# Performance work log

Measured on AMD Instinct MI355X. Metric: run time of the kernel, lower is better.

Reference implementation:

```python
import jax, jax.numpy as jnp
import numpy as np

T, B, IN, H = 512, 64, 256, 1024
LN_EPS = 1e-5


def _uniform(key, shape, fan_in):
    bound = 1.0 / np.sqrt(fan_in)
    return jax.random.uniform(key, shape, jnp.float32, -bound, bound)


def setup_inputs() -> dict:
    key = jax.random.key(0)
    ks = jax.random.split(key, 8)
    return {
        "x": jax.random.normal(ks[0], (T, B, IN), jnp.float32),
        "Wproj": _uniform(ks[1], (IN, H), IN),          # input_projection (no bias)
        "Wx0": _uniform(ks[2], (IN, 4 * H), IN),        # layer-0 input weights
        "Wh0": _uniform(ks[3], (H, 4 * H), H),          # layer-0 hidden weights
        "b0": _uniform(ks[4], (4 * H,), H),             # combined input+hidden bias
        "Wx1": _uniform(ks[5], (H, 4 * H), H),
        "Wh1": _uniform(ks[6], (H, 4 * H), H),
        "b1": _uniform(ks[7], (4 * H,), H),
        # per-layer LayerNorm params: [num_layers=2, H]
        "lnc_g": jnp.ones((2, H), jnp.float32), "lnc_b": jnp.zeros((2, H), jnp.float32),
        "lnh_g": jnp.ones((2, H), jnp.float32), "lnh_b": jnp.zeros((2, H), jnp.float32),
        "lno_g": jnp.ones((2, H), jnp.float32), "lno_b": jnp.zeros((2, H), jnp.float32),
    }


def _ln(v, g, b):
    m = jnp.mean(v, axis=-1, keepdims=True)
    var = jnp.mean((v - m) ** 2, axis=-1, keepdims=True)
    return (v - m) * jax.lax.rsqrt(var + LN_EPS) * g + b


def reference(x, Wproj, Wx0, Wh0, b0, Wx1, Wh1, b1,
              lnc_g, lnc_b, lnh_g, lnh_b, lno_g, lno_b):
    def cell(inp, h, c, Wx, Wh, bias, l):
        gates = inp @ Wx + h @ Wh + bias            # [B, 4H]
        i, f, g, o = jnp.split(gates, 4, axis=-1)
        c = jax.nn.sigmoid(f) * c + jnp.exp(i) * jnp.tanh(g)  # exponential input gate
        c = _ln(c, lnc_g[l], lnc_b[l])
        h = jax.nn.sigmoid(o) * jnp.tanh(c)
        h = _ln(h, lnh_g[l], lnh_b[l])
        return h, c

    def step(carry, xt):
        h0, c0, h1, c1 = carry
        # layer 0: cell -> residual (projected input) -> outer LayerNorm
        h0, c0 = cell(xt, h0, c0, Wx0, Wh0, b0, 0)
        h0 = _ln(h0 + xt @ Wproj, lno_g[0], lno_b[0])
        # layer 1: cell -> identity residual -> outer LayerNorm
        h1, c1 = cell(h0, h1, c1, Wx1, Wh1, b1, 1)
        h1 = _ln(h1 + h0, lno_g[1], lno_b[1])
        return (h0, c0, h1, c1), h1

    z = jnp.zeros((x.shape[1], H), x.dtype)
    (h0, c0, h1, c1), output = jax.lax.scan(step, (z, z, z, z), x)
    h_final = jnp.stack([h0, h1])  # [num_layers, B, H]
    c_final = jnp.stack([c0, c1])
    return output, h_final, c_final
```

## Files before the change

kernel.cpp:

```cpp
#include <hip/hip_runtime.h>
#include <math.h>

#define TSTEPS 512
#define BSZ    64
#define INDIM  256
#define HDIM   1024
#define G4     4096
#define NX     5120
#define LN_EPS 1e-5f

#define NBLK   256
#define NTHR   1024
#define CHUNK  8
#define CROWS  (CHUNK * BSZ)
#define NCHUNK (TSTEPS / CHUNK)
#define HRING  16
#define HSLOT  65536

#define LDS_LDK    2054
#define LDS_LO_OFF (16 * LDS_LDK)
#define LDS_W_BYTES (2 * 16 * LDS_LDK * 2)
#define LDS_STG_OFF LDS_W_BYTES
#define LDS_RED_OFF (LDS_W_BYTES + 4096)
#define LDS_BYTES   (LDS_W_BYTES + 4096 + 256)

typedef short          s8v __attribute__((ext_vector_type(8)));
typedef float          f4v __attribute__((ext_vector_type(4)));
typedef unsigned short u16;

#define MFMA __builtin_amdgcn_mfma_f32_16x16x32_bf16

__device__ __forceinline__ u16 f2bf(float f) {
    unsigned u = __float_as_uint(f);
    u += 0x7FFFu + ((u >> 16) & 1u);
    return (u16)(u >> 16);
}
__device__ __forceinline__ float bf2f(u16 h) {
    return __uint_as_float(((unsigned)h) << 16);
}
__device__ __forceinline__ float sigm(float x) { return 1.f / (1.f + expf(-x)); }

__device__ __forceinline__ float aldf(const float* p) {
    unsigned v = __hip_atomic_load((unsigned*)p, __ATOMIC_RELAXED,
                                   __HIP_MEMORY_SCOPE_AGENT);
    return __uint_as_float(v);
}
__device__ __forceinline__ void astf(float* p, float v) {
    __hip_atomic_store((unsigned*)p, __float_as_uint(v), __ATOMIC_RELAXED,
                       __HIP_MEMORY_SCOPE_AGENT);
}
__device__ __forceinline__ void ast16B(u16* p, s8v v) {
    asm volatile("global_store_dwordx4 %0, %1, off sc1"
                 :: "v"(p), "v"(v) : "memory");
}

#define GSTRIDE 512
__device__ __forceinline__ void grid_barrier(int* bar, int nbar, bool fence)
{
    asm volatile("s_waitcnt vmcnt(0)" ::: "memory");
    __syncthreads();
    if (threadIdx.x == 0) {
        const int blk = blockIdx.x;
        const int g   = blk & 15;
        int* gctr = bar + g * GSTRIDE;
        int* ggo  = gctr + 32;
        int* root = bar + 16 * GSTRIDE;
        int v = __hip_atomic_fetch_add(gctr, 1, __ATOMIC_RELAXED,
                                       __HIP_MEMORY_SCOPE_AGENT);
        if (v == nbar * 16 - 1)
            __hip_atomic_fetch_add(root, 1, __ATOMIC_RELAXED,
                                   __HIP_MEMORY_SCOPE_AGENT);
        if (blk < 16) {
            while (__hip_atomic_load(root, __ATOMIC_RELAXED,
                                     __HIP_MEMORY_SCOPE_AGENT) < nbar * 16) {}
            __hip_atomic_store(ggo, nbar, __ATOMIC_RELAXED,
                               __HIP_MEMORY_SCOPE_AGENT);
        } else {
            while (__hip_atomic_load(ggo, __ATOMIC_RELAXED,
                                     __HIP_MEMORY_SCOPE_AGENT) < nbar) {}
        }
        if (fence)
            __builtin_amdgcn_fence(__ATOMIC_ACQUIRE, "agent");
        asm volatile("" ::: "memory");
    }
    __syncthreads();
}

__device__ __forceinline__ void taskA(int g, int lane,
    const u16* __restrict__ h0hi_s, const u16* __restrict__ h0lo_s,
    const u16* __restrict__ Whthi, const u16* __restrict__ Whtlo,
    float* __restrict__ parts0)
{
    const int ks = g & 1, tile = g >> 1;
    const int rt = tile & 3, ct = tile >> 2;
    const int row = lane & 15, kg = lane >> 4;
    const int m = rt * 16 + row;
    const u16* wh = Whthi + (size_t)(ct * 16 + row) * HDIM + ks * 512 + kg * 8;
    const u16* wl = Whtlo + (size_t)(ct * 16 + row) * HDIM + ks * 512 + kg * 8;
    const u16* ah = h0hi_s + (size_t)m * HDIM + ks * 512 + kg * 8;
    const u16* al = h0lo_s + (size_t)m * HDIM + ks * 512 + kg * 8;
    f4v acc = {0.f, 0.f, 0.f, 0.f};
    s8v Ah = *(const s8v*)(ah);
    s8v Al = *(const s8v*)(al);
    s8v Bh = *(const s8v*)(wh);
    s8v Bl = *(const s8v*)(wl);
#pragma unroll
    for (int i = 0; i < 16; ++i) {
        s8v nAh, nAl, nBh, nBl;
        if (i + 1 < 16) {
            const int kn = (i + 1) * 32;
            nAh = *(const s8v*)(ah + kn);
            nAl = *(const s8v*)(al + kn);
            nBh = *(const s8v*)(wh + kn);
            nBl = *(const s8v*)(wl + kn);
        }
        acc = MFMA(Ah, Bh, acc, 0, 0, 0);
        acc = MFMA(Ah, Bl, acc, 0, 0, 0);
        acc = MFMA(Al, Bh, acc, 0, 0, 0);
        Ah = nAh; Al = nAl; Bh = nBh; Bl = nBl;
    }
    float* Cp = parts0 + (size_t)ks * BSZ * G4;
#pragma unroll
    for (int r = 0; r < 4; ++r)
        astf(&Cp[(size_t)(rt * 16 + kg * 4 + r) * G4 + ct * 16 + row], acc[r]);
}

__device__ __forceinline__ void taskX(int task, int c, int lane,
    const u16* __restrict__ xhi, const u16* __restrict__ xlo,
    const u16* __restrict__ Wxthi, const u16* __restrict__ Wxtlo,
    float* __restrict__ xgbuf)
{
    const int mt = task & 31, ct = task >> 5;
    const int row = lane & 15, kg = lane >> 4;
    const int mr = mt * 16 + row;
    const u16* ah = xhi + ((size_t)c * CROWS + mr) * INDIM + kg * 8;
    const u16* al = xlo + ((size_t)c * CROWS + mr) * INDIM + kg * 8;
    const u16* wh = Wxthi + (size_t)(ct * 16 + row) * INDIM + kg * 8;
    const u16* wl = Wxtlo + (size_t)(ct * 16 + row) * INDIM + kg * 8;
    f4v acc = {0.f, 0.f, 0.f, 0.f};
    s8v Ah = *(const s8v*)(ah);
    s8v Al = *(const s8v*)(al);
    s8v Bh = *(const s8v*)(wh);
    s8v Bl = *(const s8v*)(wl);
#pragma unroll
    for (int i = 0; i < 8; ++i) {
        s8v nAh, nAl, nBh, nBl;
        if (i + 1 < 8) {
            const int kn = (i + 1) * 32;
            nAh = *(const s8v*)(ah + kn);
            nAl = *(const s8v*)(al + kn);
            nBh = *(const s8v*)(wh + kn);
            nBl = *(const s8v*)(wl + kn);
        }
        acc = MFMA(Ah, Bh, acc, 0, 0, 0);
        acc = MFMA(Ah, Bl, acc, 0, 0, 0);
        acc = MFMA(Al, Bh, acc, 0, 0, 0);
        Ah = nAh; Al = nAl; Bh = nBh; Bl = nBl;
    }
#pragma unroll
    for (int r = 0; r < 4; ++r)
        astf(&xgbuf[(size_t)(mt * 16 + kg * 4 + r) * NX + ct * 16 + row], acc[r]);
}

__device__ __forceinline__ void taskC(int blk, int wv, int lane,
    const u16* __restrict__ shW,
    const u16* __restrict__ h0hi_s, const u16* __restrict__ h0lo_s,
    const u16* __restrict__ h1hi_s, const u16* __restrict__ h1lo_s,
    float* __restrict__ parts1)
{
    const int rt = wv & 3, hs = wv >> 2;
    const int row = lane & 15, kg = lane >> 4;
    const int m = rt * 16 + row;
    const u16* ah0 = (hs ? h1hi_s : h0hi_s) + (size_t)m * HDIM + kg * 8;
    const u16* al0 = (hs ? h1lo_s : h0lo_s) + (size_t)m * HDIM + kg * 8;
    const u16* sh  = shW + row * LDS_LDK + hs * 1024 + kg * 8;
    const u16* sl  = shW + LDS_LO_OFF + row * LDS_LDK + hs * 1024 + kg * 8;
    f4v acc = {0.f, 0.f, 0.f, 0.f};
    s8v Ah = *(const s8v*)(ah0);
    s8v Al = *(const s8v*)(al0);
#pragma unroll
    for (int i = 0; i < 32; ++i) {
        s8v nAh, nAl;
        if (i + 1 < 32) {
            nAh = *(const s8v*)(ah0 + (i + 1) * 32);
            nAl = *(const s8v*)(al0 + (i + 1) * 32);
        }
        const int kloc = i * 32;
        s8v Bh = *(const s8v*)(sh + kloc);
        s8v Bl = *(const s8v*)(sl + kloc);
        acc = MFMA(Ah, Bh, acc, 0, 0, 0);
        acc = MFMA(Ah, Bl, acc, 0, 0, 0);
        acc = MFMA(Al, Bh, acc, 0, 0, 0);
        Ah = nAh; Al = nAl;
    }
    float* Cp = parts1 + (size_t)hs * BSZ * G4;
#pragma unroll
    for (int r = 0; r < 4; ++r)
        astf(&Cp[(size_t)(rt * 16 + kg * 4 + r) * G4 + blk * 16 + row], acc[r]);
}

__device__ __forceinline__ float2 blk_sum2(float s, float q, float* red, int tid)
{
#pragma unroll
    for (int off = 32; off; off >>= 1) {
        s += __shfl_down(s, off);
        q += __shfl_down(q, off);
    }
    if ((tid & 63) == 0) { red[(tid >> 6) * 2] = s; red[(tid >> 6) * 2 + 1] = q; }
    __syncthreads();
    float ts = 0.f, tq = 0.f;
#pragma unroll
    for (int i = 0; i < 16; ++i) { ts += red[2 * i]; tq += red[2 * i + 1]; }
    __syncthreads();
    return make_float2(ts, tq);
}

__device__ __forceinline__ float lnorm(float v, float2 sq, float g, float b)
{
    float mean = sq.x * (1.f / 1024.f);
    float var  = sq.y * (1.f / 1024.f) - mean * mean;
    return (v - mean) * rsqrtf(var + LN_EPS) * g + b;
}

__device__ __forceinline__ void store_h_16B(u16* stg, int tid,
                                            u16 hi, u16 lo,
                                            u16* dhi, u16* dlo, int base)
{
    stg[tid] = hi;
    stg[1024 + tid] = lo;
    __syncthreads();
    if (tid < 256) {
        const u16* src = stg + (tid >> 7) * 1024 + (tid & 127) * 8;
        s8v v = *(const s8v*)src;
        u16* dst = ((tid >> 7) == 0 ? dhi : dlo) + base + (tid & 127) * 8;
        ast16B(dst, v);
    }
    __syncthreads();
}

__global__ __launch_bounds__(NTHR, 4) void persistent(
    const u16* __restrict__ xhi,  const u16* __restrict__ xlo,
    const u16* __restrict__ Whthi, const u16* __restrict__ Whtlo,
    const u16* __restrict__ Wxthi, const u16* __restrict__ Wxtlo,
    const u16* __restrict__ W1thi, const u16* __restrict__ W1tlo,
    const float* __restrict__ b0, const float* __restrict__ b1,
    const float* __restrict__ lncg, const float* __restrict__ lncb,
    const float* __restrict__ lnhg, const float* __restrict__ lnhb,
    const float* __restrict__ lnog, const float* __restrict__ lnob,
    float* __restrict__ xg,
    float* __restrict__ parts0,
    float* __restrict__ parts1,
    u16* __restrict__ h0hi, u16* __restrict__ h0lo,
    u16* __restrict__ h1hi, u16* __restrict__ h1lo,
    float* __restrict__ out, int* bar)
{
    extern __shared__ char smem[];
    u16*   shW = (u16*)smem;
    u16*   stg = (u16*)(smem + LDS_STG_OFF);
    float* red = (float*)(smem + LDS_RED_OFF);

    const int blk  = blockIdx.x;
    const int tid  = threadIdx.x;
    const int wv   = tid >> 6;
    const int lane = tid & 63;
    int nbar = 0;

    float c0reg = 0.f, h0reg = 0.f, c1reg = 0.f, h1reg = 0.f;

    {
        const size_t gcol = (size_t)(blk * 16 + wv) * 2048;
        for (int j = lane * 8; j < 2048; j += 512) {
            *(s8v*)(shW + wv * LDS_LDK + j)              = *(const s8v*)(W1thi + gcol + j);
            *(s8v*)(shW + LDS_LO_OFF + wv * LDS_LDK + j) = *(const s8v*)(W1tlo + gcol + j);
        }
    }
    grid_barrier(bar, ++nbar, false);

    {
        const int g = blk * 16 + wv;
        for (int task = g; task < 10240; task += 4096)
            taskX(task, 0, lane, xhi, xlo, Wxthi, Wxtlo, xg);
    }
    grid_barrier(bar, ++nbar, false);

    for (int t = 0; t < TSTEPS; ++t) {
        const int s0  = t & (HRING - 1);
        const int s0p = (t - 1) & (HRING - 1);
        const int s1p = (t - 1) & (HRING - 1);
        const bool fence = ((t & 7) == 7);

        if (blk < 64) {
            const int b = blk, n = tid;
            const float* XG = xg + (size_t)((t >> 3) & 1) * CROWS * NX
                                 + (size_t)((t & 7) * BSZ + b) * NX;
            const float* P0 = parts0 + (size_t)b * G4;
            const float* P1 = parts0 + (size_t)(BSZ + b) * G4;
            float gi = aldf(&XG[n])        + aldf(&P0[n])        + aldf(&P1[n])        + b0[n];
            float gf = aldf(&XG[1024 + n]) + aldf(&P0[1024 + n]) + aldf(&P1[1024 + n]) + b0[1024 + n];
            float gg = aldf(&XG[2048 + n]) + aldf(&P0[2048 + n]) + aldf(&P1[2048 + n]) + b0[2048 + n];
            float go = aldf(&XG[3072 + n]) + aldf(&P0[3072 + n]) + aldf(&P1[3072 + n]) + b0[3072 + n];
            float xp = aldf(&XG[4096 + n]);
            float cv = sigm(gf) * c0reg + expf(gi) * tanhf(gg);
            float2 r = blk_sum2(cv, cv * cv, red, tid);
            float cl = lnorm(cv, r, lncg[n], lncb[n]);
            c0reg = cl;
            float hv = sigm(go) * tanhf(cl);
            r = blk_sum2(hv, hv * hv, red, tid);
            float hl = lnorm(hv, r, lnhg[n], lnhb[n]) + xp;
            r = blk_sum2(hl, hl * hl, red, tid);
            float hn = lnorm(hl, r, lnog[n], lnob[n]);
            h0reg = hn;
            u16 hi = f2bf(hn);
            store_h_16B(stg, tid, hi, f2bf(hn - bf2f(hi)),
                        h0hi + (size_t)s0 * HSLOT, h0lo + (size_t)s0 * HSLOT,
                        b * HDIM);
        } else if (blk < 128) {
            if (t > 0) {
                const int b = blk - 64, n = tid;
                const float* P0 = parts1 + (size_t)b * G4;
                const float* P1 = parts1 + (size_t)(BSZ + b) * G4;
                float gi = aldf(&P0[n])        + aldf(&P1[n])        + b1[n];
                float gf = aldf(&P0[1024 + n]) + aldf(&P1[1024 + n]) + b1[1024 + n];
                float gg = aldf(&P0[2048 + n]) + aldf(&P1[2048 + n]) + b1[2048 + n];
                float go = aldf(&P0[3072 + n]) + aldf(&P1[3072 + n]) + b1[3072 + n];
                float cv = sigm(gf) * c1reg + expf(gi) * tanhf(gg);
                float2 r = blk_sum2(cv, cv * cv, red, tid);
                float cl = lnorm(cv, r, lncg[HDIM + n], lncb[HDIM + n]);
                c1reg = cl;
                float hv = sigm(go) * tanhf(cl);
                r = blk_sum2(hv, hv * hv, red, tid);
                float h0v = bf2f(h0hi[(size_t)s0p * HSLOT + b * HDIM + n])
                          + bf2f(h0lo[(size_t)s0p * HSLOT + b * HDIM + n]);
                float hl = lnorm(hv, r, lnhg[HDIM + n], lnhb[HDIM + n]) + h0v;
                r = blk_sum2(hl, hl * hl, red, tid);
                float hn = lnorm(hl, r, lnog[HDIM + n], lnob[HDIM + n]);
                h1reg = hn;
                u16 hi = f2bf(hn);
                out[(size_t)(t - 1) * BSZ * HDIM + b * HDIM + n] = hn;
                store_h_16B(stg, tid, hi, f2bf(hn - bf2f(hi)),
                            h1hi + (size_t)s1p * HSLOT, h1lo + (size_t)s1p * HSLOT,
                            b * HDIM);
            }
        } else if ((t & 7) == 7 && (t >> 3) + 1 < NCHUNK) {
            const int c = (t >> 3) + 1;
            float* xgbuf = xg + (size_t)(c & 1) * CROWS * NX;
            const int g = (blk - 128) * 16 + wv;
            for (int i = 0; i < 5; ++i)
                taskX(g + 2048 * i, c, lane, xhi, xlo, Wxthi, Wxtlo, xgbuf);
        }
        grid_barrier(bar, ++nbar, false);

        if (wv < 8) {
            taskC(blk, wv, lane, shW,
                  h0hi + (size_t)s0 * HSLOT,  h0lo + (size_t)s0 * HSLOT,
                  h1hi + (size_t)s1p * HSLOT, h1lo + (size_t)s1p * HSLOT,
                  parts1);
        } else if (t + 1 < TSTEPS) {
            taskA(blk * 8 + (wv - 8), lane,
                  h0hi + (size_t)s0 * HSLOT, h0lo + (size_t)s0 * HSLOT,
                  Whthi, Whtlo, parts0);
        }
        grid_barrier(bar, ++nbar, fence);
    }

    if (blk >= 64 && blk < 128) {
        const int b = blk - 64, n = tid;
        const int tp = TSTEPS - 1;
        const int sp = tp & (HRING - 1);
        const float* P0 = parts1 + (size_t)b * G4;
        const float* P1 = parts1 + (size_t)(BSZ + b) * G4;
        float gi = aldf(&P0[n])        + aldf(&P1[n])        + b1[n];
        float gf = aldf(&P0[1024 + n]) + aldf(&P1[1024 + n]) + b1[1024 + n];
        float gg = aldf(&P0[2048 + n]) + aldf(&P1[2048 + n]) + b1[2048 + n];
        float go = aldf(&P0[3072 + n]) + aldf(&P1[3072 + n]) + b1[3072 + n];
        float cv = sigm(gf) * c1reg + expf(gi) * tanhf(gg);
        float2 r = blk_sum2(cv, cv * cv, red, tid);
        float cl = lnorm(cv, r, lncg[HDIM + n], lncb[HDIM + n]);
        c1reg = cl;
        float hv = sigm(go) * tanhf(cl);
        r = blk_sum2(hv, hv * hv, red, tid);
        float h0v = bf2f(h0hi[(size_t)sp * HSLOT + b * HDIM + n])
                  + bf2f(h0lo[(size_t)sp * HSLOT + b * HDIM + n]);
        float hl = lnorm(hv, r, lnhg[HDIM + n], lnhb[HDIM + n]) + h0v;
        r = blk_sum2(hl, hl * hl, red, tid);
        float hn = lnorm(hl, r, lnog[HDIM + n], lnob[HDIM + n]);
        h1reg = hn;
        out[(size_t)tp * BSZ * HDIM + b * HDIM + n] = hn;
    }

    {
        const size_t F = (size_t)TSTEPS * BSZ * HDIM;
        if (blk < 64) {
            out[F +          blk * HDIM + tid] = h0reg;
            out[F + 131072 + blk * HDIM + tid] = c0reg;
        } else if (blk < 128) {
            const int b = blk - 64;
            out[F +  65536 + b * HDIM + tid] = h1reg;
            out[F + 196608 + b * HDIM + tid] = c1reg;
        }
    }
}

__global__ __launch_bounds__(256) void transpose_split(
    const float* __restrict__ src, int N,
    u16* __restrict__ dsthi, u16* __restrict__ dstlo,
    int ldd, int noff, int koff)
{
    __shared__ float tile[32][33];
    const int n0 = blockIdx.x * 32, k0 = blockIdx.y * 32;
    const int tx = threadIdx.x & 31, ty = threadIdx.x >> 5;
#pragma unroll
    for (int i = 0; i < 4; ++i)
        tile[ty + i * 8][tx] = src[(size_t)(k0 + ty + i * 8) * N + n0 + tx];
    __syncthreads();
#pragma unroll
    for (int i = 0; i < 4; ++i) {
        float v = tile[tx][ty + i * 8];
        u16 hi = f2bf(v);
        u16 lo = f2bf(v - bf2f(hi));
        size_t idx = (size_t)(n0 + ty + i * 8 + noff) * ldd + k0 + koff + tx;
        dsthi[idx] = hi;
        dstlo[idx] = lo;
    }
}

__global__ void conv_split(const float* __restrict__ src,
                           u16* __restrict__ hi, u16* __restrict__ lo, int n4)
{
    int i = blockIdx.x * 256 + threadIdx.x;
    if (i < n4) {
        float4 v = ((const float4*)src)[i];
        ushort4 h, l;
        h.x = f2bf(v.x); l.x = f2bf(v.x - bf2f(h.x));
        h.y = f2bf(v.y); l.y = f2bf(v.y - bf2f(h.y));
        h.z = f2bf(v.z); l.z = f2bf(v.z - bf2f(h.z));
        h.w = f2bf(v.w); l.w = f2bf(v.w - bf2f(h.w));
        ((ushort4*)hi)[i] = h;
        ((ushort4*)lo)[i] = l;
    }
}

extern "C" void kernel_launch(void* const* d_in, const int* in_sizes, int n_in,
                              void* d_out, int out_size, void* d_ws, size_t ws_size,
                              hipStream_t stream)
{
    const float* x     = (const float*)d_in[0];
    const float* Wproj = (const float*)d_in[1];
    const float* Wx0   = (const float*)d_in[2];
    const float* Wh0   = (const float*)d_in[3];
    const float* b0    = (const float*)d_in[4];
    const float* Wx1   = (const float*)d_in[5];
    const float* Wh1   = (const float*)d_in[6];
    const float* b1    = (const float*)d_in[7];
    const float* lnc_g = (const float*)d_in[8];
    const float* lnc_b = (const float*)d_in[9];
    const float* lnh_g = (const float*)d_in[10];
    const float* lnh_b = (const float*)d_in[11];
    const float* lno_g = (const float*)d_in[12];
    const float* lno_b = (const float*)d_in[13];
    float* out = (float*)d_out;

    char* base = (char*)d_ws;
    size_t o = 0;
    u16* x_hi  = (u16*)(base + o); o += (size_t)TSTEPS * BSZ * INDIM * 2;
    u16* x_lo  = (u16*)(base + o); o += (size_t)TSTEPS * BSZ * INDIM * 2;
    u16* Whthi = (u16*)(base + o); o += (size_t)G4 * HDIM * 2;
    u16* Whtlo = (u16*)(base + o); o += (size_t)G4 * HDIM * 2;
    u16* Wxthi = (u16*)(base + o); o += (size_t)NX * INDIM * 2;
    u16* Wxtlo = (u16*)(base + o); o += (size_t)NX * INDIM * 2;
    u16* W1thi = (u16*)(base + o); o += (size_t)G4 * 2048 * 2;
    u16* W1tlo = (u16*)(base + o); o += (size_t)G4 * 2048 * 2;
    float* xg     = (float*)(base + o); o += (size_t)2 * CROWS * NX * 4;
    float* parts0 = (float*)(base + o); o += (size_t)2 * BSZ * G4 * 4;
    float* parts1 = (float*)(base + o); o += (size_t)2 * BSZ * G4 * 4;
    u16* h0hi = (u16*)(base + o); o += (size_t)HRING * HSLOT * 2;
    u16* h0lo = (u16*)(base + o); o += (size_t)HRING * HSLOT * 2;
    u16* h1hi = (u16*)(base + o); o += (size_t)HRING * HSLOT * 2;
    u16* h1lo = (u16*)(base + o); o += (size_t)HRING * HSLOT * 2;
    int* bar  = (int*)(base + o); o += 40960;
    if (ws_size < o) return;

    conv_split<<<dim3(8192), 256, 0, stream>>>(x, x_hi, x_lo, 2097152);
    transpose_split<<<dim3(128, 32), 256, 0, stream>>>(Wh0, G4, Whthi, Whtlo, HDIM, 0, 0);
    transpose_split<<<dim3(128, 8),  256, 0, stream>>>(Wx0,   G4,   Wxthi, Wxtlo, INDIM, 0,    0);
    transpose_split<<<dim3(32, 8),   256, 0, stream>>>(Wproj, HDIM, Wxthi, Wxtlo, INDIM, 4096, 0);
    transpose_split<<<dim3(128, 32), 256, 0, stream>>>(Wx1, G4, W1thi, W1tlo, 2048, 0, 0);
    transpose_split<<<dim3(128, 32), 256, 0, stream>>>(Wh1, G4, W1thi, W1tlo, 2048, 0, 1024);
    hipMemsetAsync(parts0, 0, (size_t)2 * BSZ * G4 * 4, stream);
    hipMemsetAsync(h0hi, 0, (size_t)4 * HRING * HSLOT * 2, stream);
    hipMemsetAsync(bar, 0, 40960, stream);

    persistent<<<dim3(NBLK), dim3(NTHR), LDS_BYTES, stream>>>(
        x_hi, x_lo, Whthi, Whtlo, Wxthi, Wxtlo, W1thi, W1tlo, b0, b1,
        lnc_g, lnc_b, lnh_g, lnh_b, lno_g, lno_b,
        xg, parts0, parts1,
        h0hi, h0lo, h1hi, h1lo, out, bar);
}
```

Baseline: 25.69 ms.

## Spread input-gate GEMM across steps, vectorize C stores, flatten grid barrier

The input-projection GEMM for the next chunk used to run only on every eighth step. It is now spread evenly over all eight steps, so no single step carries the whole load before its barrier. MFMA accumulator tiles are staged through a per-wave LDS buffer and written as 16-byte stores instead of four scalar atomic stores per lane. The grid barrier now has the last arriving block set all 16 group release flags directly, which removes the extra hop through the 16 leader blocks. In exchange it uses 16 KB more LDS and a non-atomic staging round trip whose visibility relies on the sc1 stores.

```diff
diff --git a/kernel.cpp b/kernel.cpp
--- a/kernel.cpp
+++ b/kernel.cpp
@@ -22,7 +22,8 @@
 #define LDS_W_BYTES (2 * 16 * LDS_LDK * 2)
 #define LDS_STG_OFF LDS_W_BYTES
 #define LDS_RED_OFF (LDS_W_BYTES + 4096)
-#define LDS_BYTES   (LDS_W_BYTES + 4096 + 256)
+#define LDS_GST_OFF (LDS_RED_OFF + 256)
+#define LDS_BYTES   (LDS_GST_OFF + 16384)
 
 typedef short          s8v __attribute__((ext_vector_type(8)));
 typedef float          f4v __attribute__((ext_vector_type(4)));
@@ -45,14 +46,25 @@
                                    __HIP_MEMORY_SCOPE_AGENT);
     return __uint_as_float(v);
 }
-__device__ __forceinline__ void astf(float* p, float v) {
-    __hip_atomic_store((unsigned*)p, __float_as_uint(v), __ATOMIC_RELAXED,
-                       __HIP_MEMORY_SCOPE_AGENT);
-}
 __device__ __forceinline__ void ast16B(u16* p, s8v v) {
     asm volatile("global_store_dwordx4 %0, %1, off sc1"
                  :: "v"(p), "v"(v) : "memory");
 }
+__device__ __forceinline__ void ast16Bf(float* p, f4v v) {
+    asm volatile("global_store_dwordx4 %0, %1, off sc1"
+                 :: "v"(p), "v"(v) : "memory");
+}
+
+__device__ __forceinline__ void store_c_16B(float* stgw, int lane, f4v acc,
+                                            float* dst, int ld)
+{
+    const int row = lane & 15, kg = lane >> 4;
+#pragma unroll
+    for (int r = 0; r < 4; ++r)
+        stgw[(kg * 4 + r) * 16 + row] = acc[r];
+    f4v v = *(f4v*)(stgw + lane * 4);
+    ast16Bf(dst + (lane >> 2) * ld + (lane & 3) * 4, v);
+}
 
 #define GSTRIDE 512
 __device__ __forceinline__ void grid_barrier(int* bar, int nbar, bool fence)
@@ -60,25 +72,24 @@
     asm volatile("s_waitcnt vmcnt(0)" ::: "memory");
     __syncthreads();
     if (threadIdx.x == 0) {
-        const int blk = blockIdx.x;
-        const int g   = blk & 15;
+        const int g = blockIdx.x & 15;
         int* gctr = bar + g * GSTRIDE;
         int* ggo  = gctr + 32;
         int* root = bar + 16 * GSTRIDE;
         int v = __hip_atomic_fetch_add(gctr, 1, __ATOMIC_RELAXED,
                                        __HIP_MEMORY_SCOPE_AGENT);
-        if (v == nbar * 16 - 1)
-            __hip_atomic_fetch_add(root, 1, __ATOMIC_RELAXED,
-                                   __HIP_MEMORY_SCOPE_AGENT);
-        if (blk < 16) {
-            while (__hip_atomic_load(root, __ATOMIC_RELAXED,
-                                     __HIP_MEMORY_SCOPE_AGENT) < nbar * 16) {}
-            __hip_atomic_store(ggo, nbar, __ATOMIC_RELAXED,
-                               __HIP_MEMORY_SCOPE_AGENT);
-        } else {
-            while (__hip_atomic_load(ggo, __ATOMIC_RELAXED,
-                                     __HIP_MEMORY_SCOPE_AGENT) < nbar) {}
-        }
+        if (v == nbar * 16 - 1) {
+            int rv = __hip_atomic_fetch_add(root, 1, __ATOMIC_RELAXED,
+                                            __HIP_MEMORY_SCOPE_AGENT);
+            if (rv == nbar * 16 - 1) {
+#pragma unroll
+                for (int g2 = 0; g2 < 16; ++g2)
+                    __hip_atomic_store(bar + g2 * GSTRIDE + 32, nbar,
+                                       __ATOMIC_RELAXED, __HIP_MEMORY_SCOPE_AGENT);
+            }
+        }
+        while (__hip_atomic_load(ggo, __ATOMIC_RELAXED,
+                                 __HIP_MEMORY_SCOPE_AGENT) < nbar) {}
         if (fence)
             __builtin_amdgcn_fence(__ATOMIC_ACQUIRE, "agent");
         asm volatile("" ::: "memory");
@@ -86,7 +97,7 @@
     __syncthreads();
 }
 
-__device__ __forceinline__ void taskA(int g, int lane,
+__device__ __forceinline__ void taskA(int g, int lane, float* stgw,
     const u16* __restrict__ h0hi_s, const u16* __restrict__ h0lo_s,
     const u16* __restrict__ Whthi, const u16* __restrict__ Whtlo,
     float* __restrict__ parts0)
@@ -119,13 +130,12 @@
         acc = MFMA(Al, Bh, acc, 0, 0, 0);
         Ah = nAh; Al = nAl; Bh = nBh; Bl = nBl;
     }
-    float* Cp = parts0 + (size_t)ks * BSZ * G4;
-#pragma unroll
-    for (int r = 0; r < 4; ++r)
-        astf(&Cp[(size_t)(rt * 16 + kg * 4 + r) * G4 + ct * 16 + row], acc[r]);
-}
-
-__device__ __forceinline__ void taskX(int task, int c, int lane,
+    store_c_16B(stgw, lane, acc,
+                parts0 + (size_t)ks * BSZ * G4 + (size_t)(rt * 16) * G4 + ct * 16,
+                G4);
+}
+
+__device__ __forceinline__ void taskX(int task, int c, int lane, float* stgw,
     const u16* __restrict__ xhi, const u16* __restrict__ xlo,
     const u16* __restrict__ Wxthi, const u16* __restrict__ Wxtlo,
     float* __restrict__ xgbuf)
@@ -157,12 +167,11 @@
         acc = MFMA(Al, Bh, acc, 0, 0, 0);
         Ah = nAh; Al = nAl; Bh = nBh; Bl = nBl;
     }
-#pragma unroll
-    for (int r = 0; r < 4; ++r)
-        astf(&xgbuf[(size_t)(mt * 16 + kg * 4 + r) * NX + ct * 16 + row], acc[r]);
-}
-
-__device__ __forceinline__ void taskC(int blk, int wv, int lane,
+    store_c_16B(stgw, lane, acc,
+                xgbuf + (size_t)(mt * 16) * NX + ct * 16, NX);
+}
+
+__device__ __forceinline__ void taskC(int blk, int wv, int lane, float* stgw,
     const u16* __restrict__ shW,
     const u16* __restrict__ h0hi_s, const u16* __restrict__ h0lo_s,
     const u16* __restrict__ h1hi_s, const u16* __restrict__ h1lo_s,
@@ -193,10 +202,9 @@
         acc = MFMA(Al, Bh, acc, 0, 0, 0);
         Ah = nAh; Al = nAl;
     }
-    float* Cp = parts1 + (size_t)hs * BSZ * G4;
-#pragma unroll
-    for (int r = 0; r < 4; ++r)
-        astf(&Cp[(size_t)(rt * 16 + kg * 4 + r) * G4 + blk * 16 + row], acc[r]);
+    store_c_16B(stgw, lane, acc,
+                parts1 + (size_t)hs * BSZ * G4 + (size_t)(rt * 16) * G4 + blk * 16,
+                G4);
 }
 
 __device__ __forceinline__ float2 blk_sum2(float s, float q, float* red, int tid)
@@ -255,14 +263,16 @@
     float* __restrict__ out, int* bar)
 {
     extern __shared__ char smem[];
-    u16*   shW = (u16*)smem;
-    u16*   stg = (u16*)(smem + LDS_STG_OFF);
-    float* red = (float*)(smem + LDS_RED_OFF);
+    u16*   shW   = (u16*)smem;
+    u16*   stg   = (u16*)(smem + LDS_STG_OFF);
+    float* red   = (float*)(smem + LDS_RED_OFF);
+    float* stg_g = (float*)(smem + LDS_GST_OFF);
 
     const int blk  = blockIdx.x;
     const int tid  = threadIdx.x;
     const int wv   = tid >> 6;
     const int lane = tid & 63;
+    float* stgw = stg_g + wv * 256;
     int nbar = 0;
 
     float c0reg = 0.f, h0reg = 0.f, c1reg = 0.f, h1reg = 0.f;
@@ -279,7 +289,7 @@
     {
         const int g = blk * 16 + wv;
         for (int task = g; task < 10240; task += 4096)
-            taskX(task, 0, lane, xhi, xlo, Wxthi, Wxtlo, xg);
+            taskX(task, 0, lane, stgw, xhi, xlo, Wxthi, Wxtlo, xg);
     }
     grid_barrier(bar, ++nbar, false);
 
@@ -341,22 +351,25 @@
                             h1hi + (size_t)s1p * HSLOT, h1lo + (size_t)s1p * HSLOT,
                             b * HDIM);
             }
-        } else if ((t & 7) == 7 && (t >> 3) + 1 < NCHUNK) {
+        } else {
             const int c = (t >> 3) + 1;
-            float* xgbuf = xg + (size_t)(c & 1) * CROWS * NX;
-            const int g = (blk - 128) * 16 + wv;
-            for (int i = 0; i < 5; ++i)
-                taskX(g + 2048 * i, c, lane, xhi, xlo, Wxthi, Wxtlo, xgbuf);
+            if (c < NCHUNK) {
+                float* xgbuf = xg + (size_t)(c & 1) * CROWS * NX;
+                const int widx = (blk - 128) * 16 + wv;
+                if (widx < 1280)
+                    taskX((t & 7) * 1280 + widx, c, lane, stgw,
+                          xhi, xlo, Wxthi, Wxtlo, xgbuf);
+            }
         }
         grid_barrier(bar, ++nbar, false);
 
         if (wv < 8) {
-            taskC(blk, wv, lane, shW,
+            taskC(blk, wv, lane, stgw, shW,
                   h0hi + (size_t)s0 * HSLOT,  h0lo + (size_t)s0 * HSLOT,
                   h1hi + (size_t)s1p * HSLOT, h1lo + (size_t)s1p * HSLOT,
                   parts1);
         } else if (t + 1 < TSTEPS) {
-            taskA(blk * 8 + (wv - 8), lane,
+            taskA(blk * 8 + (wv - 8), lane, stgw,
                   h0hi + (size_t)s0 * HSLOT, h0lo + (size_t)s0 * HSLOT,
                   Whthi, Whtlo, parts0);
         }
```

Result: no change. 25.35 ms (-1.3%).
